# Kernel optimization log

Measured on AMD Instinct MI355X. Metric: run time of the kernel, lower is better.

The kernel has to match this reference:

```python
import jax, jax.numpy as jnp
import numpy as np

B, L, H, A, T, E = 8192, 128, 256, 32, 65, 8


def setup_inputs() -> dict:
    key = jax.random.key(0)
    ks = jax.random.split(key, 17)
    n = lambda i, shape: jax.random.normal(ks[i], shape, dtype=jnp.float32) * 0.05
    return dict(
        latent=jax.random.normal(ks[0], (B, L), dtype=jnp.float32),
        target=jax.random.randint(ks[1], (B, T), 0, A),
        embed=n(2, (A, E)),
        W_ih=n(3, (3 * H, E)), b_ih=n(4, (3 * H,)),
        W_hh=n(5, (3 * H, H)), b_hh=n(6, (3 * H,)),
        Wd0=n(7, (L, H)), bd0=n(8, (H,)),
        Wd1=n(9, (H, H)), bd1=n(10, (H,)),
        Wd2=n(11, (H, H)), bd2=n(12, (H,)),
        Wp1=n(13, (H, A)), bp1=n(14, (A,)),
        Wp2=n(15, (A, A)), bp2=n(16, (A,)),
    )


def reference(latent, target, embed, W_ih, b_ih, W_hh, b_hh,
              Wd0, bd0, Wd1, bd1, Wd2, bd2, Wp1, bp1, Wp2, bp2):
    # Latent -> initial GRU hidden (Dropout is identity at inference)
    h = jax.nn.relu(latent @ Wd0 + bd0)
    h = jax.nn.relu(h @ Wd1 + bd1)
    h = h @ Wd2 + bd2  # [B, H]

    # Teacher forcing: step i consumes token 0 (start) then target[:, i-1]
    start = jnp.zeros((target.shape[0], 1), dtype=target.dtype)
    tokens = jnp.concatenate([start, target[:, :-1]], axis=1)  # [B, T]
    x = embed[tokens]                                          # [B, T, E]
    xs = jnp.swapaxes(x, 0, 1)                                 # [T, B, E] time-major

    def gru_step(h, x_t):
        gi = x_t @ W_ih.T + b_ih   # [B, 3H]
        gh = h @ W_hh.T + b_hh     # [B, 3H]
        ir, iz, i_n = jnp.split(gi, 3, axis=-1)
        hr, hz, h_n = jnp.split(gh, 3, axis=-1)
        r = jax.nn.sigmoid(ir + hr)
        z = jax.nn.sigmoid(iz + hz)
        n = jnp.tanh(i_n + r * h_n)
        h_new = (1.0 - z) * n + z * h
        return h_new, h_new

    _, hs = jax.lax.scan(gru_step, h, xs)              # hs: [T, B, H]
    logits = jax.nn.relu(hs @ Wp1 + bp1) @ Wp2 + bp2   # [T, B, A]
    return jnp.swapaxes(logits, 0, 1)                  # [B, T, A]
```

## Files before the change

kernel.cpp:

```cpp
#include <hip/hip_runtime.h>
#include <hip/hip_fp16.h>

#define B_  8192
#define L_  128
#define H_  256
#define A_  32
#define T_  65
#define BM  16

typedef _Float16 f16x8 __attribute__((ext_vector_type(8)));
typedef _Float16 f16x4 __attribute__((ext_vector_type(4)));
typedef float    f32x4 __attribute__((ext_vector_type(4)));

static __device__ __forceinline__ float sigm(float x) {
  return __builtin_amdgcn_rcpf(1.f + __expf(-x));
}
static __device__ __forceinline__ float tanh_f(float x) {
  return 1.f - 2.f * __builtin_amdgcn_rcpf(1.f + __expf(2.f * x));
}

static __device__ __forceinline__ uint32_t hoff(int m, uint32_t byte_in_row) {
  return (uint32_t)(m * 512) + (byte_in_row ^ (uint32_t)((m & 7) << 4));
}

static __device__ __forceinline__ f16x8 ldFrag(const _Float16* buf, int row, int g, int kt) {
  return *(const f16x8*)((const char*)buf + hoff(row, (uint32_t)(kt * 64 + g * 16)));
}
static __device__ __forceinline__ void stH(_Float16* buf, int m, int c, float v) {
  *(_Float16*)((char*)buf + hoff(m, 2u * (uint32_t)c)) = (_Float16)v;
}


__global__ void prep_convert(const float* __restrict__ latent, const float* __restrict__ Whh,
                             _Float16* __restrict__ latent16, _Float16* __restrict__ Whh16) {
  const int tid = blockIdx.x * blockDim.x + threadIdx.x;
  const int stride = gridDim.x * blockDim.x;
  for (int i = tid; i < B_ * L_; i += stride) latent16[i] = (_Float16)latent[i];
  for (int i = tid; i < 768 * H_; i += stride) Whh16[i] = (_Float16)Whh[i];
}

__global__ void prep_transpose(const float* __restrict__ Wd0, const float* __restrict__ Wd1,
                               const float* __restrict__ Wd2, const float* __restrict__ Wp1,
                               const float* __restrict__ Wp2,
                               _Float16* __restrict__ Wd0T, _Float16* __restrict__ Wd1T,
                               _Float16* __restrict__ Wd2T, _Float16* __restrict__ Wp1T,
                               _Float16* __restrict__ Wp2T) {
  const int tid = blockIdx.x * blockDim.x + threadIdx.x;
  const int stride = gridDim.x * blockDim.x;
  for (int i = tid; i < 256 * 128; i += stride) { int n = i / 128, k = i % 128; Wd0T[i] = (_Float16)Wd0[k * 256 + n]; }
  for (int i = tid; i < 256 * 256; i += stride) { int n = i / 256, k = i % 256; Wd1T[i] = (_Float16)Wd1[k * 256 + n]; }
  for (int i = tid; i < 256 * 256; i += stride) { int n = i / 256, k = i % 256; Wd2T[i] = (_Float16)Wd2[k * 256 + n]; }
  for (int i = tid; i < 32 * 256;  i += stride) { int n = i / 256, k = i % 256; Wp1T[i] = (_Float16)Wp1[k * 32 + n]; }
  for (int i = tid; i < 32 * 32;   i += stride) { int n = i / 32,  k = i % 32;  Wp2T[i] = (_Float16)Wp2[k * 32 + n]; }
}

__global__ void prep_g4(const float* __restrict__ embed, const float* __restrict__ W_ih,
                        const float* __restrict__ b_ih, const float* __restrict__ b_hh,
                        _Float16* __restrict__ G4) {
  const int idx = blockIdx.x * blockDim.x + threadIdx.x;
  if (idx >= A_ * 256 * 4) return;
  const int j = idx & 3, c = (idx >> 2) & 255, a = idx >> 10;
  if (j == 3) { G4[idx] = (_Float16)0.f; return; }
  const int cc = j * 256 + c;
  float s = b_ih[cc] + (j < 2 ? b_hh[cc] : 0.f);
#pragma unroll
  for (int e = 0; e < 8; ++e) s += embed[a * 8 + e] * W_ih[cc * 8 + e];
  G4[idx] = (_Float16)s;
}


__global__ __launch_bounds__(256, 1) void decoder_main(
    const _Float16* __restrict__ latent16, const int* __restrict__ target,
    const _Float16* __restrict__ Whh16, const _Float16* __restrict__ G4,
    const _Float16* __restrict__ Wd0T, const _Float16* __restrict__ Wd1T,
    const _Float16* __restrict__ Wd2T, const _Float16* __restrict__ Wp1T,
    const _Float16* __restrict__ Wp2T,
    const float* __restrict__ bd0, const float* __restrict__ bd1, const float* __restrict__ bd2,
    const float* __restrict__ b_hh, const float* __restrict__ bp1, const float* __restrict__ bp2,
    float* __restrict__ out) {
  __shared__ _Float16 hbuf[2][BM * 256];
  __shared__ int      tok_lds[BM * T_];
  __shared__ _Float16 o1_lds[BM * 40];

  const int tid = threadIdx.x;
  const int w  = tid >> 6;
  const int l  = tid & 63;
  const int lo = l & 15;
  const int g  = l >> 4;
  const int b0 = blockIdx.x * BM;

  for (int i = tid; i < BM * T_; i += 256) {
    const int m = i / T_, t = i % T_;
    tok_lds[i] = (t == 0) ? 0 : target[(size_t)(b0 + m) * T_ + (t - 1)];
  }

  float hold[4][4];

  {
    f16x8 af[4];
#pragma unroll
    for (int kt = 0; kt < 4; ++kt)
      af[kt] = *(const f16x8*)(latent16 + (size_t)(b0 + lo) * 128 + kt * 32 + g * 8);
    f32x4 acc[4] = {};
#pragma unroll
    for (int q = 0; q < 4; ++q) {
      const _Float16* bb = Wd0T + (size_t)(w * 64 + q * 16 + lo) * 128 + g * 8;
#pragma unroll
      for (int kt = 0; kt < 4; ++kt) {
        f16x8 bf = *(const f16x8*)(bb + kt * 32);
        acc[q] = __builtin_amdgcn_mfma_f32_16x16x32_f16(af[kt], bf, acc[q], 0, 0, 0);
      }
    }
#pragma unroll
    for (int q = 0; q < 4; ++q) {
      const int n = w * 64 + q * 16 + lo;
      const float bv = bd0[n];
#pragma unroll
      for (int i = 0; i < 4; ++i)
        stH(hbuf[0], 4 * g + i, n, fmaxf(acc[q][i] + bv, 0.f));
    }
  }
  __syncthreads();
  {
    f16x8 af[8];
#pragma unroll
    for (int kt = 0; kt < 8; ++kt) af[kt] = ldFrag(hbuf[0], lo, g, kt);
    f32x4 acc[4] = {};
#pragma unroll
    for (int q = 0; q < 4; ++q) {
      const _Float16* bb = Wd1T + (size_t)(w * 64 + q * 16 + lo) * 256 + g * 8;
#pragma unroll
      for (int kt = 0; kt < 8; ++kt) {
        f16x8 bf = *(const f16x8*)(bb + kt * 32);
        acc[q] = __builtin_amdgcn_mfma_f32_16x16x32_f16(af[kt], bf, acc[q], 0, 0, 0);
      }
    }
#pragma unroll
    for (int q = 0; q < 4; ++q) {
      const int n = w * 64 + q * 16 + lo;
      const float bv = bd1[n];
#pragma unroll
      for (int i = 0; i < 4; ++i)
        stH(hbuf[1], 4 * g + i, n, fmaxf(acc[q][i] + bv, 0.f));
    }
  }
  __syncthreads();
  {
    f16x8 af[8];
#pragma unroll
    for (int kt = 0; kt < 8; ++kt) af[kt] = ldFrag(hbuf[1], lo, g, kt);
    f32x4 acc[4] = {};
#pragma unroll
    for (int q = 0; q < 4; ++q) {
      const _Float16* bb = Wd2T + (size_t)(w * 64 + q * 16 + lo) * 256 + g * 8;
#pragma unroll
      for (int kt = 0; kt < 8; ++kt) {
        f16x8 bf = *(const f16x8*)(bb + kt * 32);
        acc[q] = __builtin_amdgcn_mfma_f32_16x16x32_f16(af[kt], bf, acc[q], 0, 0, 0);
      }
    }
    __syncthreads();
#pragma unroll
    for (int q = 0; q < 4; ++q) {
      const int n = w * 64 + q * 16 + lo;
      const float bv = bd2[n];
#pragma unroll
      for (int i = 0; i < 4; ++i) {
        const float hv = acc[q][i] + bv;
        stH(hbuf[0], 4 * g + i, n, hv);
        hold[i][q] = hv;
      }
    }
  }
  __syncthreads();

  f16x8 wr[12][8];
#pragma unroll
  for (int gt = 0; gt < 3; ++gt)
#pragma unroll
    for (int q = 0; q < 4; ++q)
#pragma unroll
      for (int kt = 0; kt < 8; ++kt)
        wr[gt * 4 + q][kt] =
            *(const f16x8*)(Whh16 + (size_t)(gt * 256 + w * 64 + q * 16 + lo) * 256 + kt * 32 + g * 8);

  float bhn[4];
#pragma unroll
  for (int q = 0; q < 4; ++q) bhn[q] = b_hh[512 + w * 64 + q * 16 + lo];
  const int at = w;
  float bp1v = 0.f, bp2v = 0.f;
  if (w < 2) { bp1v = bp1[at * 16 + lo]; bp2v = bp2[at * 16 + lo]; }

#pragma unroll 1
  for (int t = 0; t < T_; ++t) {
    const _Float16* hr = hbuf[t & 1];
    _Float16* hw = hbuf[(t & 1) ^ 1];

    int tk[4];
#pragma unroll
    for (int i = 0; i < 4; ++i) tk[i] = tok_lds[(4 * g + i) * T_ + t];

    f16x4 gvp[4][4];
#pragma unroll
    for (int i = 0; i < 4; ++i) {
      const _Float16* Grow = G4 + (size_t)tk[i] * 1024;
#pragma unroll
      for (int q = 0; q < 4; ++q)
        gvp[i][q] = *(const f16x4*)(Grow + (w * 64 + q * 16 + lo) * 4);
    }

    f16x8 af[8];
#pragma unroll
    for (int kt = 0; kt < 8; ++kt) af[kt] = ldFrag(hr, lo, g, kt);

#pragma unroll
    for (int q = 0; q < 4; ++q) {
      f32x4 a3[3];
#pragma unroll
      for (int gt = 0; gt < 3; ++gt) a3[gt] = (f32x4){0.f, 0.f, 0.f, 0.f};
#pragma unroll
      for (int gt = 0; gt < 3; ++gt)
#pragma unroll
        for (int kt = 0; kt < 8; ++kt)
          a3[gt] = __builtin_amdgcn_mfma_f32_16x16x32_f16(af[kt], wr[gt * 4 + q][kt], a3[gt], 0, 0, 0);

      const int c = w * 64 + q * 16 + lo;
#pragma unroll
      for (int i = 0; i < 4; ++i) {
        const float r = sigm(a3[0][i] + (float)gvp[i][q][0]);
        const float z = sigm(a3[1][i] + (float)gvp[i][q][1]);
        const float nn = tanh_f((float)gvp[i][q][2] + r * (a3[2][i] + bhn[q]));
        const float hv = nn + z * (hold[i][q] - nn);
        hold[i][q] = hv;
        stH(hw, 4 * g + i, c, hv);
      }
    }
    __syncthreads();

    if (w < 2) {
      f32x4 accp = {};
#pragma unroll
      for (int kt = 0; kt < 8; ++kt) {
        f16x8 a1 = ldFrag(hw, lo, g, kt);
        f16x8 b1 = *(const f16x8*)(Wp1T + (size_t)(at * 16 + lo) * 256 + kt * 32 + g * 8);
        accp = __builtin_amdgcn_mfma_f32_16x16x32_f16(a1, b1, accp, 0, 0, 0);
      }
      const int ac = at * 16 + lo;
#pragma unroll
      for (int i = 0; i < 4; ++i)
        o1_lds[(4 * g + i) * 40 + ac] = (_Float16)fmaxf(accp[i] + bp1v, 0.f);
    }
    __syncthreads();
    if (w < 2) {
      f16x8 a2 = *(const f16x8*)(o1_lds + lo * 40 + g * 8);
      f16x8 b2 = *(const f16x8*)(Wp2T + (at * 16 + lo) * 32 + g * 8);
      f32x4 accl = {};
      accl = __builtin_amdgcn_mfma_f32_16x16x32_f16(a2, b2, accl, 0, 0, 0);
#pragma unroll
      for (int i = 0; i < 4; ++i) {
        const int m = 4 * g + i;
        out[((size_t)(b0 + m) * T_ + t) * A_ + at * 16 + lo] = accl[i] + bp2v;
      }
    }
  }
}


extern "C" void kernel_launch(void* const* d_in, const int* in_sizes, int n_in,
                              void* d_out, int out_size, void* d_ws, size_t ws_size,
                              hipStream_t stream) {
  const float* latent = (const float*)d_in[0];
  const int*   target = (const int*)d_in[1];
  const float* embed  = (const float*)d_in[2];
  const float* W_ih   = (const float*)d_in[3];
  const float* b_ih   = (const float*)d_in[4];
  const float* W_hh   = (const float*)d_in[5];
  const float* b_hh   = (const float*)d_in[6];
  const float* Wd0    = (const float*)d_in[7];
  const float* bd0    = (const float*)d_in[8];
  const float* Wd1    = (const float*)d_in[9];
  const float* bd1    = (const float*)d_in[10];
  const float* Wd2    = (const float*)d_in[11];
  const float* bd2    = (const float*)d_in[12];
  const float* Wp1    = (const float*)d_in[13];
  const float* bp1    = (const float*)d_in[14];
  const float* Wp2    = (const float*)d_in[15];
  const float* bp2    = (const float*)d_in[16];
  float* out = (float*)d_out;

  char* ws = (char*)d_ws;
  size_t off = 0;
  auto carve = [&](size_t bytes) { char* p = ws + off; off += (bytes + 255) & ~(size_t)255; return p; };
  _Float16* latent16 = (_Float16*)carve((size_t)B_ * L_ * 2);
  _Float16* Whh16    = (_Float16*)carve((size_t)768 * H_ * 2);
  _Float16* Wd0T     = (_Float16*)carve(256 * 128 * 2);
  _Float16* Wd1T     = (_Float16*)carve(256 * 256 * 2);
  _Float16* Wd2T     = (_Float16*)carve(256 * 256 * 2);
  _Float16* Wp1T     = (_Float16*)carve(32 * 256 * 2);
  _Float16* Wp2T     = (_Float16*)carve(32 * 32 * 2);
  _Float16* G4       = (_Float16*)carve(A_ * 256 * 4 * 2);

  prep_convert<<<1024, 256, 0, stream>>>(latent, W_hh, latent16, Whh16);
  prep_transpose<<<256, 256, 0, stream>>>(Wd0, Wd1, Wd2, Wp1, Wp2, Wd0T, Wd1T, Wd2T, Wp1T, Wp2T);
  prep_g4<<<(A_ * 256 * 4 + 255) / 256, 256, 0, stream>>>(embed, W_ih, b_ih, b_hh, G4);
  decoder_main<<<B_ / BM, 256, 0, stream>>>(latent16, target, Whh16, G4,
                                            Wd0T, Wd1T, Wd2T, Wp1T, Wp2T,
                                            bd0, bd1, bd2, b_hh, bp1, bp2, out);
}
```

Before: 587.0 us.

## Pipeline output projection across waves and drop one barrier per step

Double-buffers the first projection layer's activations in LDS. Waves 0-1 compute the first projection layer for step t while waves 2-3 compute the second layer and store logits for step t-1, with a final epilogue for the last step. This removes one __syncthreads per timestep and spreads the projection work over all four waves instead of two. It also keeps the Wp2 fragment in registers, at the cost of some extra LDS and register use.

```diff
diff --git a/kernel.cpp b/kernel.cpp
--- a/kernel.cpp
+++ b/kernel.cpp
@@ -80,7 +80,7 @@
     float* __restrict__ out) {
   __shared__ _Float16 hbuf[2][BM * 256];
   __shared__ int      tok_lds[BM * T_];
-  __shared__ _Float16 o1_lds[BM * 40];
+  __shared__ _Float16 o1_lds[2][BM * 40];
 
   const int tid = threadIdx.x;
   const int w  = tid >> 6;
@@ -187,9 +187,16 @@
   float bhn[4];
 #pragma unroll
   for (int q = 0; q < 4; ++q) bhn[q] = b_hh[512 + w * 64 + q * 16 + lo];
-  const int at = w;
+  const int at1 = w;
+  const int at2 = w - 2;
   float bp1v = 0.f, bp2v = 0.f;
-  if (w < 2) { bp1v = bp1[at * 16 + lo]; bp2v = bp2[at * 16 + lo]; }
+  f16x8 wp2f = {};
+  if (w < 2) {
+    bp1v = bp1[at1 * 16 + lo];
+  } else {
+    bp2v = bp2[at2 * 16 + lo];
+    wp2f = *(const f16x8*)(Wp2T + (at2 * 16 + lo) * 32 + g * 8);
+  }
 
 #pragma unroll 1
   for (int t = 0; t < T_; ++t) {
@@ -242,26 +249,31 @@
 #pragma unroll
       for (int kt = 0; kt < 8; ++kt) {
         f16x8 a1 = ldFrag(hw, lo, g, kt);
-        f16x8 b1 = *(const f16x8*)(Wp1T + (size_t)(at * 16 + lo) * 256 + kt * 32 + g * 8);
+        f16x8 b1 = *(const f16x8*)(Wp1T + (size_t)(at1 * 16 + lo) * 256 + kt * 32 + g * 8);
         accp = __builtin_amdgcn_mfma_f32_16x16x32_f16(a1, b1, accp, 0, 0, 0);
       }
-      const int ac = at * 16 + lo;
+      const int ac = at1 * 16 + lo;
 #pragma unroll
       for (int i = 0; i < 4; ++i)
-        o1_lds[(4 * g + i) * 40 + ac] = (_Float16)fmaxf(accp[i] + bp1v, 0.f);
-    }
-    __syncthreads();
-    if (w < 2) {
-      f16x8 a2 = *(const f16x8*)(o1_lds + lo * 40 + g * 8);
-      f16x8 b2 = *(const f16x8*)(Wp2T + (at * 16 + lo) * 32 + g * 8);
+        o1_lds[t & 1][(4 * g + i) * 40 + ac] = (_Float16)fmaxf(accp[i] + bp1v, 0.f);
+    } else if (t > 0) {
+      f16x8 a2 = *(const f16x8*)(o1_lds[(t - 1) & 1] + lo * 40 + g * 8);
       f32x4 accl = {};
-      accl = __builtin_amdgcn_mfma_f32_16x16x32_f16(a2, b2, accl, 0, 0, 0);
-#pragma unroll
-      for (int i = 0; i < 4; ++i) {
-        const int m = 4 * g + i;
-        out[((size_t)(b0 + m) * T_ + t) * A_ + at * 16 + lo] = accl[i] + bp2v;
-      }
-    }
+      accl = __builtin_amdgcn_mfma_f32_16x16x32_f16(a2, wp2f, accl, 0, 0, 0);
+#pragma unroll
+      for (int i = 0; i < 4; ++i)
+        out[((size_t)(b0 + 4 * g + i) * T_ + (t - 1)) * A_ + at2 * 16 + lo] = accl[i] + bp2v;
+    }
+  }
+
+  __syncthreads();
+  if (w >= 2) {
+    f16x8 a2 = *(const f16x8*)(o1_lds[(T_ - 1) & 1] + lo * 40 + g * 8);
+    f32x4 accl = {};
+    accl = __builtin_amdgcn_mfma_f32_16x16x32_f16(a2, wp2f, accl, 0, 0, 0);
+#pragma unroll
+    for (int i = 0; i < 4; ++i)
+      out[((size_t)(b0 + 4 * g + i) * T_ + (T_ - 1)) * A_ + at2 * 16 + lo] = accl[i] + bp2v;
   }
 }
 
```

Result: no change. 592.6 us (+1.0%).
